# Optimization experiments

Measured on AMD Instinct MI355X. Metric: run time of the kernel, lower is better.

The kernel has to match this reference:

```python
import jax, jax.numpy as jnp
import numpy as np

N, E, NFEAT, NHID, NCLASS = 50000, 800000, 8, 128, 112
SMOOTH = 0.5          # smoo init arg
NEG_SLOPE_ATT = 0.2   # LeakyReLU slope inside sparse attention (SpGAT convention)
NEG_SLOPE_OUT = 0.01  # F.leaky_relu default in the outer loop
EPS = 1e-16


def setup_inputs() -> dict:
    key = jax.random.key(0)
    ks = jax.random.split(key, 12)
    g = lambda k, shape, s=0.1: jax.random.normal(k, shape, dtype=jnp.float32) * s
    return {
        "x": jax.random.normal(ks[0], (N, NFEAT), dtype=jnp.float32),
        "edge_index": jax.random.randint(ks[1], (2, E), 0, N, dtype=jnp.int64) if jax.config.jax_enable_x64 else jax.random.randint(ks[1], (2, E), 0, N, dtype=jnp.int32),
        "edge_weight": jax.random.uniform(ks[2], (E,), dtype=jnp.float32),
        # ScattterAttentionLayer 1: nfeat -> nhid (weight W, attention vector a split into src/dst halves)
        "W1": g(ks[3], (NFEAT, NHID)),
        "a1_src": g(ks[4], (NHID,)),
        "a1_dst": g(ks[5], (NHID,)),
        # ScattterAttentionLayer 2: nhid -> nhid
        "W2": g(ks[6], (NHID, NHID)),
        "a2_src": g(ks[7], (NHID,)),
        "a2_dst": g(ks[8], (NHID,)),
        # shared BatchNorm1d(nhid)
        "gamma": jnp.ones((NHID,), jnp.float32),
        "beta": jnp.zeros((NHID,), jnp.float32),
        # GC_withres: nhid -> nclass
        "Wg": g(ks[9], (NHID, NCLASS)),
        "bg": jnp.zeros((NCLASS,), jnp.float32),
    }


def scatter_attention(h_in, W, a_src, a_dst, src, dst):
    """Sparse GAT-style scatter attention (SpGraphAttentionLayer math).
    score_ij = exp(-leakyrelu(a_src.h_i + a_dst.h_j)); softmax-normalized per dst node."""
    h = h_in @ W                                   # [N, F]
    f_src = h @ a_src                              # [N]
    f_dst = h @ a_dst                              # [N]
    e = jnp.exp(-jax.nn.leaky_relu(f_src[src] + f_dst[dst], NEG_SLOPE_ATT))  # [E]
    denom = jax.ops.segment_sum(e, dst, num_segments=N) + EPS                # [N]
    num = jax.ops.segment_sum(e[:, None] * h[src], dst, num_segments=N)      # [N, F]
    return num / denom[:, None]


def batchnorm(x, gamma, beta):
    mu = x.mean(axis=0)
    var = x.var(axis=0)
    return (x - mu) * jax.lax.rsqrt(var + 1e-5) * gamma + beta


def reference(x, edge_index, edge_weight, W1, a1_src, a1_dst, W2, a2_src, a2_dst, gamma, beta, Wg, bg):
    src, dst = edge_index[0], edge_index[1]
    # conv loop (nlayers=3 -> two ScattterAttentionLayer convs), shared bn1, leaky_relu; dropout=identity (eval)
    h = scatter_attention(x, W1, a1_src, a1_dst, src, dst)
    h = jax.nn.leaky_relu(batchnorm(h, gamma, beta), NEG_SLOPE_OUT)
    h = scatter_attention(h, W2, a2_src, a2_dst, src, dst)
    h = jax.nn.leaky_relu(batchnorm(h, gamma, beta), NEG_SLOPE_OUT)
    # GC_withres: spmm((smooth*A + I)/(1+smooth), h @ Wg) + bias
    support = h @ Wg                               # [N, nclass]
    w = (SMOOTH / (1.0 + SMOOTH)) * edge_weight    # [E]
    agg = jax.ops.segment_sum(w[:, None] * support[src], dst, num_segments=N)
    return agg + support / (1.0 + SMOOTH) + bg
```

## Files before the change

kernel.cpp:

```cpp
#include <hip/hip_runtime.h>
#include <hip/hip_bf16.h>

#define N_NODES 50000
#define N_EDGES 800000
#define NFEAT   8
#define NHID    128
#define NCLASS  112
#define SEG_EPS 1e-16f
#define BN_EPS  1e-5f
#define CAP     64
#define MACRO_TILES 782
#define STAT_ROWS 50
#define STAT_BLOCKS 1000
#define NODE_RANGE 6250
#define FILL_CHUNK 2048
#define FILL_CHUNKS 391

typedef __hip_bfloat16 bf16;
typedef __attribute__((ext_vector_type(8))) short short8;
typedef __attribute__((ext_vector_type(4))) float f32x4;

__device__ __forceinline__ float bfbits2f(unsigned int lo16) {
    union { unsigned int u; float f; } c; c.u = lo16 << 16; return c.f;
}

__global__ __launch_bounds__(256)
void k_fill_bucket(const int* __restrict__ src, const int* __restrict__ dst,
                   const float* __restrict__ ewt,
                   int* __restrict__ cnt, unsigned int* __restrict__ bucket) {
    const int range = blockIdx.x & 7;
    const int chunk = blockIdx.x >> 3;
    const int lo = range * NODE_RANGE, hi = lo + NODE_RANGE;
    const int e0 = chunk * FILL_CHUNK + threadIdx.x;
#pragma unroll
    for (int i = 0; i < 8; i++) {
        int e = e0 + i * 256;
        if (e >= N_EDGES) break;
        int d = dst[e];
        if (d < lo || d >= hi) continue;
        int slot = atomicAdd(&cnt[d], 1);
        if (slot < CAP) {
            unsigned int iw = (unsigned int)(ewt[e] * 32767.f + 0.5f);
            bucket[d * CAP + slot] = ((unsigned int)src[e] << 15) | iw;
        }
    }
}

__global__ __launch_bounds__(256)
void k_sort_bucket(const int* __restrict__ cnt, unsigned int* __restrict__ bucket) {
    int d = blockIdx.x * 4 + (threadIdx.x >> 6);
    int lane = threadIdx.x & 63;
    int deg = min(cnt[d], CAP);
    unsigned int v = (lane < deg) ? bucket[d * CAP + lane] : 0xFFFFFFFFu;
#pragma unroll
    for (int k = 2; k <= 64; k <<= 1) {
#pragma unroll
        for (int s = k >> 1; s > 0; s >>= 1) {
            unsigned int o = (unsigned int)__shfl_xor((int)v, s);
            bool keepmin = ((lane & s) == 0) == ((lane & k) == 0);
            v = keepmin ? min(v, o) : max(v, o);
        }
    }
    if (lane < deg) bucket[d * CAP + lane] = v;
}

__global__ void k_w1proj(const float* __restrict__ W1,
                         const float* __restrict__ a1s, const float* __restrict__ a1d,
                         float* __restrict__ w1s, float* __restrict__ w1d) {
    int w = threadIdx.x >> 6, lane = threadIdx.x & 63;
    int k = w & 7;
    const float* a = (w < 8) ? a1s : a1d;
    float v = W1[k * NHID + lane] * a[lane] + W1[k * NHID + 64 + lane] * a[64 + lane];
#pragma unroll
    for (int off = 32; off > 0; off >>= 1) v += __shfl_down(v, off);
    if (lane == 0) ((w < 8) ? w1s : w1d)[k] = v;
}

__global__ void k_fsfd(const float* __restrict__ x,
                       const float* __restrict__ w1s, const float* __restrict__ w1d,
                       float* __restrict__ fs, float* __restrict__ fd) {
    int i = blockIdx.x * 256 + threadIdx.x;
    if (i >= N_NODES) return;
    const float4 x0 = ((const float4*)x)[i * 2];
    const float4 x1 = ((const float4*)x)[i * 2 + 1];
    fs[i] = x0.x*w1s[0] + x0.y*w1s[1] + x0.z*w1s[2] + x0.w*w1s[3]
          + x1.x*w1s[4] + x1.y*w1s[5] + x1.z*w1s[6] + x1.w*w1s[7];
    fd[i] = x0.x*w1d[0] + x0.y*w1d[1] + x0.z*w1d[2] + x0.w*w1d[3]
          + x1.x*w1d[4] + x1.y*w1d[5] + x1.z*w1d[6] + x1.w*w1d[7];
}

__global__ void k_gather_x(const int* __restrict__ cnt, const unsigned int* __restrict__ bucket,
                           const float* __restrict__ fs, const float* __restrict__ fd,
                           const float* __restrict__ x, float* __restrict__ xaggn) {
    int d = blockIdx.x * 4 + (threadIdx.x >> 6);
    int lane = threadIdx.x & 63;
    int col = lane & 7, eslot = lane >> 3;
    int dg = min(cnt[d], CAP);
    float fdd = fd[d];
    float acc = 0.f, den = 0.f;
    for (int base = 0; base < dg; base += 8) {
        int e = base + eslot;
        if (e < dg) {
            int s = bucket[d * CAP + e] >> 15;
            float f = fs[s] + fdd;
            float lr = f > 0.f ? f : 0.2f * f;
            float c = __expf(-lr);
            den += c;
            acc += c * x[s * NFEAT + col];
        }
    }
#pragma unroll
    for (int off = 8; off < 64; off <<= 1) {
        acc += __shfl_xor(acc, off);
        den += __shfl_xor(den, off);
    }
    if (eslot == 0) xaggn[d * NFEAT + col] = acc / (den + SEG_EPS);
}

__global__ __launch_bounds__(256)
void k_y1_gemm(const float* __restrict__ xaggn, const float* __restrict__ W1,
               bf16* __restrict__ y1, float* __restrict__ Psum, float* __restrict__ Psq) {
    int t = threadIdx.x;
    int r = t >> 7, j = t & 127;
    float w[NFEAT];
#pragma unroll
    for (int k = 0; k < NFEAT; k++) w[k] = W1[k * NHID + j];
    float ls = 0.f, lq = 0.f;
    for (int row = blockIdx.x * 2 + r; row < N_NODES; row += gridDim.x * 2) {
        const float4 x0 = ((const float4*)xaggn)[row * 2];
        const float4 x1 = ((const float4*)xaggn)[row * 2 + 1];
        float v = x0.x*w[0] + x0.y*w[1] + x0.z*w[2] + x0.w*w[3]
                + x1.x*w[4] + x1.y*w[5] + x1.z*w[6] + x1.w*w[7];
        y1[(size_t)row * NHID + j] = __float2bfloat16(v);
        ls += v; lq += v * v;
    }
    __shared__ float sbuf[256];
    sbuf[t] = ls; __syncthreads();
    if (r == 0) Psum[blockIdx.x * 128 + j] = sbuf[j] + sbuf[j + 128];
    __syncthreads();
    sbuf[t] = lq; __syncthreads();
    if (r == 0) Psq[blockIdx.x * 128 + j] = sbuf[j] + sbuf[j + 128];
}

__global__ __launch_bounds__(128)
void k_bn_stats_part(const bf16* __restrict__ y,
                     float* __restrict__ Psum, float* __restrict__ Psq) {
    int j = threadIdx.x;
    int i0 = blockIdx.x * STAT_ROWS;
    float ls = 0.f, lq = 0.f;
    for (int i = i0; i < i0 + STAT_ROWS; i++) {
        float v = __bfloat162float(y[(size_t)i * NHID + j]);
        ls += v; lq += v * v;
    }
    Psum[blockIdx.x * 128 + j] = ls;
    Psq[blockIdx.x * 128 + j] = lq;
}

__global__ __launch_bounds__(256)
void k_reduce_a(const float* __restrict__ Psum, const float* __restrict__ Psq,
                int nIn, int chunk,
                float* __restrict__ Qsum, float* __restrict__ Qsq) {
    int j = threadIdx.x & 127;
    int h = threadIdx.x >> 7;
    int u = blockIdx.x * 2 + h;
    int b0 = u * chunk, b1 = min(b0 + chunk, nIn);
    float s = 0.f, q = 0.f;
#pragma unroll 8
    for (int b = b0; b < b1; b++) {
        s += Psum[b * 128 + j];
        q += Psq[b * 128 + j];
    }
    Qsum[u * 128 + j] = s;
    Qsq[u * 128 + j] = q;
}

__global__ __launch_bounds__(512)
void k_reduce_b(const float* __restrict__ Qsum, const float* __restrict__ Qsq,
                const float* __restrict__ gamma, const float* __restrict__ beta,
                float* __restrict__ scale, float* __restrict__ shift) {
    int j = threadIdx.x & 127;
    int g = threadIdx.x >> 7;
    float s = 0.f, q = 0.f;
#pragma unroll
    for (int u = g * 8; u < g * 8 + 8; u++) {
        s += Qsum[u * 128 + j];
        q += Qsq[u * 128 + j];
    }
    __shared__ float Ls[4][128], Lq[4][128];
    Ls[g][j] = s; Lq[g][j] = q;
    __syncthreads();
    if (g == 0) {
        float st = ((Ls[0][j] + Ls[1][j]) + Ls[2][j]) + Ls[3][j];
        float qt = ((Lq[0][j] + Lq[1][j]) + Lq[2][j]) + Lq[3][j];
        float mu = st * (1.f / N_NODES);
        float var = qt * (1.f / N_NODES) - mu * mu;
        float rs = rsqrtf(var + BN_EPS);
        float ga = gamma[j];
        scale[j] = rs * ga;
        shift[j] = beta[j] - mu * rs * ga;
    }
}

__global__ void k_w2proj(const float* __restrict__ W2,
                         const float* __restrict__ as_, const float* __restrict__ ad_,
                         float* __restrict__ ws_, float* __restrict__ wd_) {
    int k = blockIdx.x, n = threadIdx.x;
    float w = W2[k * NHID + n];
    float vs = w * as_[n], vd = w * ad_[n];
#pragma unroll
    for (int off = 32; off > 0; off >>= 1) { vs += __shfl_down(vs, off); vd += __shfl_down(vd, off); }
    __shared__ float ps[2], pd[2];
    if ((n & 63) == 0) { ps[n >> 6] = vs; pd[n >> 6] = vd; }
    __syncthreads();
    if (n == 0) { ws_[k] = ps[0] + ps[1]; wd_[k] = pd[0] + pd[1]; }
}

template<int NCV, bool ATT>
__global__ __launch_bounds__(256)
void k_gemm_mfma(const bf16* __restrict__ Yin,
                 const float* __restrict__ scale, const float* __restrict__ shift,
                 const float* __restrict__ W,
                 bf16* __restrict__ hout,
                 const float* __restrict__ w2s, const float* __restrict__ w2d,
                 float* __restrict__ fs, float* __restrict__ fd) {
    constexpr int NT = NCV / 16;
    __shared__ bf16 Wt[128 * 136];
    __shared__ bf16 At[64 * 136];
    const int t = threadIdx.x;
    for (int idx = t; idx < 128 * NCV; idx += 256) {
        int k = idx / NCV, n = idx - k * NCV;
        Wt[n * 136 + k] = __float2bfloat16(W[idx]);
    }
    const int p  = t & 63;
    const int rg = t >> 6;
    const float sc0 = scale[2*p],   sh0 = shift[2*p];
    const float sc1 = scale[2*p+1], sh1 = shift[2*p+1];
    float ws0, ws1, wd0, wd1;
    if (ATT) { ws0 = w2s[2*p]; ws1 = w2s[2*p+1]; wd0 = w2d[2*p]; wd1 = w2d[2*p+1]; }
    const int lane = t & 63;
    const int m16 = lane & 15;
    const int g = lane >> 4;
    __syncthreads();

    for (int mt = blockIdx.x; mt < MACRO_TILES; mt += gridDim.x) {
        const int row0 = mt * 64;
#pragma unroll
        for (int i2 = 0; i2 < 16; i2++) {
            int row = rg + i2 * 4;
            int grow = row0 + row;
            unsigned int u = (grow < N_NODES) ? ((const unsigned int*)Yin)[(size_t)grow * 64 + p] : 0u;
            float v0 = bfbits2f(u & 0xFFFF) * sc0 + sh0; v0 = v0 > 0.f ? v0 : 0.01f * v0;
            float v1 = bfbits2f(u >> 16)    * sc1 + sh1; v1 = v1 > 0.f ? v1 : 0.01f * v1;
            union { unsigned int u; bf16 b[2]; } pk;
            pk.b[0] = __float2bfloat16(v0);
            pk.b[1] = __float2bfloat16(v1);
            *(unsigned int*)&At[row * 136 + 2 * p] = pk.u;
            if (ATT) {
                float vs = v0 * ws0 + v1 * ws1;
                float vd = v0 * wd0 + v1 * wd1;
#pragma unroll
                for (int off = 32; off > 0; off >>= 1) {
                    vs += __shfl_xor(vs, off);
                    vd += __shfl_xor(vd, off);
                }
                if (p == 0 && grow < N_NODES) { fs[grow] = vs; fd[grow] = vd; }
            }
        }
        __syncthreads();
        f32x4 acc[NT];
#pragma unroll
        for (int c = 0; c < NT; c++) acc[c] = (f32x4){0.f, 0.f, 0.f, 0.f};
#pragma unroll
        for (int kk = 0; kk < 4; kk++) {
            short8 af = *(const short8*)&At[(rg * 16 + m16) * 136 + kk * 32 + g * 8];
#pragma unroll
            for (int c = 0; c < NT; c++) {
                short8 bfr = *(const short8*)&Wt[(c * 16 + m16) * 136 + kk * 32 + g * 8];
                acc[c] = __builtin_amdgcn_mfma_f32_16x16x32_bf16(af, bfr, acc[c], 0, 0, 0);
            }
        }
        const int orow = row0 + rg * 16 + g * 4;
#pragma unroll
        for (int c = 0; c < NT; c++) {
#pragma unroll
            for (int r = 0; r < 4; r++) {
                int grow = orow + r;
                if (grow < N_NODES)
                    hout[(size_t)grow * NCV + c * 16 + m16] = __float2bfloat16(acc[c][r]);
            }
        }
        __syncthreads();
    }
}

__global__ __launch_bounds__(256)
void k_gather_attn_bf(const int* __restrict__ cnt, const unsigned int* __restrict__ bucket,
                      const float* __restrict__ fs, const float* __restrict__ fd,
                      const bf16* __restrict__ h, bf16* __restrict__ y) {
    int q = threadIdx.x >> 6;
    int j = threadIdx.x & 63;
    int d = blockIdx.x * 4 + q;
    __shared__ int s_idx[4][CAP];
    __shared__ float s_e[4][CAP];
    int deg = min(cnt[d], CAP);
    float fdd = fd[d];
    if (j < deg) {
        int s = bucket[d * CAP + j] >> 15;
        float f = fs[s] + fdd;
        float lr = f > 0.f ? f : 0.2f * f;
        s_idx[q][j] = s;
        s_e[q][j] = __expf(-lr);
    }
    __syncthreads();
    float n0 = 0.f, n1 = 0.f, den = 0.f;
#pragma unroll 4
    for (int k = 0; k < deg; k++) {
        float e = s_e[q][k];
        unsigned int u = *(const unsigned int*)&h[(size_t)s_idx[q][k] * NHID + 2 * j];
        den += e;
        n0 += e * bfbits2f(u & 0xFFFF);
        n1 += e * bfbits2f(u >> 16);
    }
    float rs = 1.f / (den + SEG_EPS);
    union { unsigned int u; bf16 b[2]; } pk;
    pk.b[0] = __float2bfloat16(n0 * rs);
    pk.b[1] = __float2bfloat16(n1 * rs);
    ((unsigned int*)y)[(size_t)d * 64 + j] = pk.u;
}

__global__ __launch_bounds__(256)
void k_gather_out_bf(const int* __restrict__ cnt, const unsigned int* __restrict__ bucket,
                     const bf16* __restrict__ sup, const float* __restrict__ bg,
                     float* __restrict__ out) {
    int q = threadIdx.x >> 6;
    int j = threadIdx.x & 63;
    int d = blockIdx.x * 4 + q;
    __shared__ int s_idx[4][CAP];
    __shared__ float s_w[4][CAP];
    int deg = min(cnt[d], CAP);
    if (j < deg) {
        unsigned int b = bucket[d * CAP + j];
        s_idx[q][j] = b >> 15;
        s_w[q][j] = (float)(b & 0x7FFF) * (1.f / (32767.f * 3.f));
    }
    __syncthreads();
    if (j >= NCLASS / 2) return;
    float a0 = 0.f, a1 = 0.f;
#pragma unroll 4
    for (int k = 0; k < deg; k++) {
        float w = s_w[q][k];
        unsigned int u = *(const unsigned int*)&sup[(size_t)s_idx[q][k] * NCLASS + 2 * j];
        a0 += w * bfbits2f(u & 0xFFFF);
        a1 += w * bfbits2f(u >> 16);
    }
    unsigned int us = *(const unsigned int*)&sup[(size_t)d * NCLASS + 2 * j];
    float2 o;
    o.x = a0 + bfbits2f(us & 0xFFFF) * (2.f / 3.f) + bg[2 * j];
    o.y = a1 + bfbits2f(us >> 16)    * (2.f / 3.f) + bg[2 * j + 1];
    *(float2*)&out[(size_t)d * NCLASS + 2 * j] = o;
}

extern "C" void kernel_launch(void* const* d_in, const int* in_sizes, int n_in,
                              void* d_out, int out_size, void* d_ws, size_t ws_size,
                              hipStream_t stream) {
    const float* x    = (const float*)d_in[0];
    const int*   ei   = (const int*)d_in[1];
    const float* ewt  = (const float*)d_in[2];
    const float* W1   = (const float*)d_in[3];
    const float* a1s  = (const float*)d_in[4];
    const float* a1d  = (const float*)d_in[5];
    const float* W2   = (const float*)d_in[6];
    const float* a2s  = (const float*)d_in[7];
    const float* a2d  = (const float*)d_in[8];
    const float* gam  = (const float*)d_in[9];
    const float* bet  = (const float*)d_in[10];
    const float* Wg   = (const float*)d_in[11];
    const float* bg   = (const float*)d_in[12];
    float* out = (float*)d_out;

    const int* src = ei;
    const int* dst = ei + N_EDGES;

    float* ws    = (float*)d_ws;
    bf16*  Yb    = (bf16*)ws;
    bf16*  Hb    = (bf16*)(ws + 3203072);
    unsigned int* bucket = (unsigned int*)(ws + 6403072);
    float* xagg  = ws + 9603072;
    float* fs    = ws + 10003072;
    float* fd    = ws + 10053072;
    int*   cnt   = (int*)(ws + 10103072);
    float* scale = ws + 10153072;
    float* shift = scale + 128;
    float* w1s   = shift + 128;
    float* w1d   = w1s + 8;
    float* w2s   = w1d + 8;
    float* w2d   = w2s + 128;
    float* Psum  = ws + 10153600;
    float* Psq   = Psum + 128000;
    float* Qsum  = Psq + 128000;
    float* Qsq   = Qsum + 4096;

    hipMemsetAsync(cnt, 0, (size_t)N_NODES * 4, stream);
    k_fill_bucket<<<FILL_CHUNKS * 8, 256, 0, stream>>>(src, dst, ewt, cnt, bucket);
    k_sort_bucket<<<N_NODES / 4, 256, 0, stream>>>(cnt, bucket);

    k_w1proj<<<1, 1024, 0, stream>>>(W1, a1s, a1d, w1s, w1d);
    k_fsfd<<<(N_NODES + 255) / 256, 256, 0, stream>>>(x, w1s, w1d, fs, fd);
    k_gather_x<<<N_NODES / 4, 256, 0, stream>>>(cnt, bucket, fs, fd, x, xagg);
    k_y1_gemm<<<256, 256, 0, stream>>>(xagg, W1, Yb, Psum, Psq);
    k_reduce_a<<<16, 256, 0, stream>>>(Psum, Psq, 256, 8, Qsum, Qsq);
    k_reduce_b<<<1, 512, 0, stream>>>(Qsum, Qsq, gam, bet, scale, shift);

    k_w2proj<<<128, 128, 0, stream>>>(W2, a2s, a2d, w2s, w2d);
    k_gemm_mfma<128, true><<<MACRO_TILES, 256, 0, stream>>>(Yb, scale, shift, W2, Hb,
                                                            w2s, w2d, fs, fd);
    k_gather_attn_bf<<<N_NODES / 4, 256, 0, stream>>>(cnt, bucket, fs, fd, Hb, Yb);
    k_bn_stats_part<<<STAT_BLOCKS, 128, 0, stream>>>(Yb, Psum, Psq);
    k_reduce_a<<<16, 256, 0, stream>>>(Psum, Psq, STAT_BLOCKS, 32, Qsum, Qsq);
    k_reduce_b<<<1, 512, 0, stream>>>(Qsum, Qsq, gam, bet, scale, shift);

    k_gemm_mfma<112, false><<<MACRO_TILES, 256, 0, stream>>>(Yb, scale, shift, Wg, Hb,
                                                             nullptr, nullptr, nullptr, nullptr);
    k_gather_out_bf<<<N_NODES / 4, 256, 0, stream>>>(cnt, bucket, Hb, bg, out);
}
```

Measured before the change: 328.3 us.

## Fuse tiny projection/BN-finalize kernels into consumers and split gather edges across half-waves

The W1 attention projection now runs inside k_fsfd and the BatchNorm finalize (k_reduce_b) runs inside each GEMM block's prologue, which removes three small serial launches. The attention and output gather kernels now have each half-wave take alternate edges with 4-wide bf16 loads, then combine the halves with a cross-lane shuffle. This gives more memory-level parallelism per node. In exchange, every GEMM block redundantly reads the 32x128 partial stats and every fsfd block recomputes the W1 projection.

Result: slower. 345.3 us (+5.2%).

```diff
diff --git a/kernel.cpp b/kernel.cpp
--- a/kernel.cpp
+++ b/kernel.cpp
@@ -64,22 +64,32 @@
     if (lane < deg) bucket[d * CAP + lane] = v;
 }
 
-__global__ void k_w1proj(const float* __restrict__ W1,
-                         const float* __restrict__ a1s, const float* __restrict__ a1d,
-                         float* __restrict__ w1s, float* __restrict__ w1d) {
-    int w = threadIdx.x >> 6, lane = threadIdx.x & 63;
-    int k = w & 7;
-    const float* a = (w < 8) ? a1s : a1d;
-    float v = W1[k * NHID + lane] * a[lane] + W1[k * NHID + 64 + lane] * a[64 + lane];
-#pragma unroll
-    for (int off = 32; off > 0; off >>= 1) v += __shfl_down(v, off);
-    if (lane == 0) ((w < 8) ? w1s : w1d)[k] = v;
-}
-
-__global__ void k_fsfd(const float* __restrict__ x,
-                       const float* __restrict__ w1s, const float* __restrict__ w1d,
-                       float* __restrict__ fs, float* __restrict__ fd) {
-    int i = blockIdx.x * 256 + threadIdx.x;
+__global__ __launch_bounds__(256)
+void k_fsfd(const float* __restrict__ W1,
+            const float* __restrict__ a1s, const float* __restrict__ a1d,
+            const float* __restrict__ x,
+            float* __restrict__ fs, float* __restrict__ fd) {
+    __shared__ float ps[8][32], pd_[8][32];
+    __shared__ float w1s[8], w1d[8];
+    int t = threadIdx.x;
+    int k = t & 7, seg = t >> 3;
+    float accs = 0.f, accd = 0.f;
+#pragma unroll
+    for (int n = seg * 4; n < seg * 4 + 4; n++) {
+        float w = W1[k * NHID + n];
+        accs += w * a1s[n];
+        accd += w * a1d[n];
+    }
+    ps[k][seg] = accs; pd_[k][seg] = accd;
+    __syncthreads();
+    if (t < 8) {
+        float vs = 0.f, vd = 0.f;
+#pragma unroll 8
+        for (int i = 0; i < 32; i++) { vs += ps[t][i]; vd += pd_[t][i]; }
+        w1s[t] = vs; w1d[t] = vd;
+    }
+    __syncthreads();
+    int i = blockIdx.x * 256 + t;
     if (i >= N_NODES) return;
     const float4 x0 = ((const float4*)x)[i * 2];
     const float4 x1 = ((const float4*)x)[i * 2 + 1];
@@ -174,33 +184,6 @@
     Qsq[u * 128 + j] = q;
 }
 
-__global__ __launch_bounds__(512)
-void k_reduce_b(const float* __restrict__ Qsum, const float* __restrict__ Qsq,
-                const float* __restrict__ gamma, const float* __restrict__ beta,
-                float* __restrict__ scale, float* __restrict__ shift) {
-    int j = threadIdx.x & 127;
-    int g = threadIdx.x >> 7;
-    float s = 0.f, q = 0.f;
-#pragma unroll
-    for (int u = g * 8; u < g * 8 + 8; u++) {
-        s += Qsum[u * 128 + j];
-        q += Qsq[u * 128 + j];
-    }
-    __shared__ float Ls[4][128], Lq[4][128];
-    Ls[g][j] = s; Lq[g][j] = q;
-    __syncthreads();
-    if (g == 0) {
-        float st = ((Ls[0][j] + Ls[1][j]) + Ls[2][j]) + Ls[3][j];
-        float qt = ((Lq[0][j] + Lq[1][j]) + Lq[2][j]) + Lq[3][j];
-        float mu = st * (1.f / N_NODES);
-        float var = qt * (1.f / N_NODES) - mu * mu;
-        float rs = rsqrtf(var + BN_EPS);
-        float ga = gamma[j];
-        scale[j] = rs * ga;
-        shift[j] = beta[j] - mu * rs * ga;
-    }
-}
-
 __global__ void k_w2proj(const float* __restrict__ W2,
                          const float* __restrict__ as_, const float* __restrict__ ad_,
                          float* __restrict__ ws_, float* __restrict__ wd_) {
@@ -218,7 +201,8 @@
 template<int NCV, bool ATT>
 __global__ __launch_bounds__(256)
 void k_gemm_mfma(const bf16* __restrict__ Yin,
-                 const float* __restrict__ scale, const float* __restrict__ shift,
+                 const float* __restrict__ Qsum, const float* __restrict__ Qsq,
+                 const float* __restrict__ gamma, const float* __restrict__ beta,
                  const float* __restrict__ W,
                  bf16* __restrict__ hout,
                  const float* __restrict__ w2s, const float* __restrict__ w2d,
@@ -233,8 +217,20 @@
     }
     const int p  = t & 63;
     const int rg = t >> 6;
-    const float sc0 = scale[2*p],   sh0 = shift[2*p];
-    const float sc1 = scale[2*p+1], sh1 = shift[2*p+1];
+    float s0 = 0.f, q0 = 0.f, s1 = 0.f, q1 = 0.f;
+#pragma unroll 8
+    for (int u = 0; u < 32; u++) {
+        s0 += Qsum[u * 128 + 2 * p];     s1 += Qsum[u * 128 + 2 * p + 1];
+        q0 += Qsq[u * 128 + 2 * p];      q1 += Qsq[u * 128 + 2 * p + 1];
+    }
+    float mu0 = s0 * (1.f / N_NODES);
+    float rs0 = rsqrtf(q0 * (1.f / N_NODES) - mu0 * mu0 + BN_EPS);
+    float g0  = gamma[2 * p];
+    const float sc0 = rs0 * g0, sh0 = beta[2 * p] - mu0 * rs0 * g0;
+    float mu1 = s1 * (1.f / N_NODES);
+    float rs1 = rsqrtf(q1 * (1.f / N_NODES) - mu1 * mu1 + BN_EPS);
+    float g1  = gamma[2 * p + 1];
+    const float sc1 = rs1 * g1, sh1 = beta[2 * p + 1] - mu1 * rs1 * g1;
     float ws0, ws1, wd0, wd1;
     if (ATT) { ws0 = w2s[2*p]; ws1 = w2s[2*p+1]; wd0 = w2d[2*p]; wd1 = w2d[2*p+1]; }
     const int lane = t & 63;
@@ -298,34 +294,39 @@
                       const float* __restrict__ fs, const float* __restrict__ fd,
                       const bf16* __restrict__ h, bf16* __restrict__ y) {
     int q = threadIdx.x >> 6;
-    int j = threadIdx.x & 63;
+    int lane = threadIdx.x & 63;
     int d = blockIdx.x * 4 + q;
     __shared__ int s_idx[4][CAP];
     __shared__ float s_e[4][CAP];
     int deg = min(cnt[d], CAP);
     float fdd = fd[d];
-    if (j < deg) {
-        int s = bucket[d * CAP + j] >> 15;
+    if (lane < deg) {
+        int s = bucket[d * CAP + lane] >> 15;
         float f = fs[s] + fdd;
         float lr = f > 0.f ? f : 0.2f * f;
-        s_idx[q][j] = s;
-        s_e[q][j] = __expf(-lr);
-    }
-    __syncthreads();
-    float n0 = 0.f, n1 = 0.f, den = 0.f;
-#pragma unroll 4
-    for (int k = 0; k < deg; k++) {
+        s_idx[q][lane] = s;
+        s_e[q][lane] = __expf(-lr);
+    }
+    __syncthreads();
+    int half = lane >> 5, j4 = lane & 31;
+    float n0 = 0.f, n1 = 0.f, n2 = 0.f, n3 = 0.f, den = 0.f;
+    for (int k = half; k < deg; k += 2) {
         float e = s_e[q][k];
-        unsigned int u = *(const unsigned int*)&h[(size_t)s_idx[q][k] * NHID + 2 * j];
+        const uint2 u = *(const uint2*)&h[(size_t)s_idx[q][k] * NHID + 4 * j4];
         den += e;
-        n0 += e * bfbits2f(u & 0xFFFF);
-        n1 += e * bfbits2f(u >> 16);
-    }
-    float rs = 1.f / (den + SEG_EPS);
-    union { unsigned int u; bf16 b[2]; } pk;
-    pk.b[0] = __float2bfloat16(n0 * rs);
-    pk.b[1] = __float2bfloat16(n1 * rs);
-    ((unsigned int*)y)[(size_t)d * 64 + j] = pk.u;
+        n0 += e * bfbits2f(u.x & 0xFFFF); n1 += e * bfbits2f(u.x >> 16);
+        n2 += e * bfbits2f(u.y & 0xFFFF); n3 += e * bfbits2f(u.y >> 16);
+    }
+    n0 += __shfl_xor(n0, 32); n1 += __shfl_xor(n1, 32);
+    n2 += __shfl_xor(n2, 32); n3 += __shfl_xor(n3, 32);
+    den += __shfl_xor(den, 32);
+    if (half == 0) {
+        float rs = 1.f / (den + SEG_EPS);
+        union { uint2 u; bf16 b[4]; } pk;
+        pk.b[0] = __float2bfloat16(n0 * rs); pk.b[1] = __float2bfloat16(n1 * rs);
+        pk.b[2] = __float2bfloat16(n2 * rs); pk.b[3] = __float2bfloat16(n3 * rs);
+        ((uint2*)y)[(size_t)d * 32 + j4] = pk.u;
+    }
 }
 
 __global__ __launch_bounds__(256)
@@ -333,31 +334,38 @@
                      const bf16* __restrict__ sup, const float* __restrict__ bg,
                      float* __restrict__ out) {
     int q = threadIdx.x >> 6;
-    int j = threadIdx.x & 63;
+    int lane = threadIdx.x & 63;
     int d = blockIdx.x * 4 + q;
     __shared__ int s_idx[4][CAP];
     __shared__ float s_w[4][CAP];
     int deg = min(cnt[d], CAP);
-    if (j < deg) {
-        unsigned int b = bucket[d * CAP + j];
-        s_idx[q][j] = b >> 15;
-        s_w[q][j] = (float)(b & 0x7FFF) * (1.f / (32767.f * 3.f));
-    }
-    __syncthreads();
-    if (j >= NCLASS / 2) return;
-    float a0 = 0.f, a1 = 0.f;
-#pragma unroll 4
-    for (int k = 0; k < deg; k++) {
-        float w = s_w[q][k];
-        unsigned int u = *(const unsigned int*)&sup[(size_t)s_idx[q][k] * NCLASS + 2 * j];
-        a0 += w * bfbits2f(u & 0xFFFF);
-        a1 += w * bfbits2f(u >> 16);
-    }
-    unsigned int us = *(const unsigned int*)&sup[(size_t)d * NCLASS + 2 * j];
-    float2 o;
-    o.x = a0 + bfbits2f(us & 0xFFFF) * (2.f / 3.f) + bg[2 * j];
-    o.y = a1 + bfbits2f(us >> 16)    * (2.f / 3.f) + bg[2 * j + 1];
-    *(float2*)&out[(size_t)d * NCLASS + 2 * j] = o;
+    if (lane < deg) {
+        unsigned int b = bucket[d * CAP + lane];
+        s_idx[q][lane] = b >> 15;
+        s_w[q][lane] = (float)(b & 0x7FFF) * (1.f / (32767.f * 3.f));
+    }
+    __syncthreads();
+    int half = lane >> 5, j4 = lane & 31;
+    float a0 = 0.f, a1 = 0.f, a2 = 0.f, a3 = 0.f;
+    if (j4 < 28) {
+        for (int k = half; k < deg; k += 2) {
+            float w = s_w[q][k];
+            const uint2 u = *(const uint2*)&sup[(size_t)s_idx[q][k] * NCLASS + 4 * j4];
+            a0 += w * bfbits2f(u.x & 0xFFFF); a1 += w * bfbits2f(u.x >> 16);
+            a2 += w * bfbits2f(u.y & 0xFFFF); a3 += w * bfbits2f(u.y >> 16);
+        }
+    }
+    a0 += __shfl_xor(a0, 32); a1 += __shfl_xor(a1, 32);
+    a2 += __shfl_xor(a2, 32); a3 += __shfl_xor(a3, 32);
+    if (half == 0 && j4 < 28) {
+        const uint2 us = *(const uint2*)&sup[(size_t)d * NCLASS + 4 * j4];
+        float4 o;
+        o.x = a0 + bfbits2f(us.x & 0xFFFF) * (2.f / 3.f) + bg[4 * j4];
+        o.y = a1 + bfbits2f(us.x >> 16)    * (2.f / 3.f) + bg[4 * j4 + 1];
+        o.z = a2 + bfbits2f(us.y & 0xFFFF) * (2.f / 3.f) + bg[4 * j4 + 2];
+        o.w = a3 + bfbits2f(us.y >> 16)    * (2.f / 3.f) + bg[4 * j4 + 3];
+        *(float4*)&out[(size_t)d * NCLASS + 4 * j4] = o;
+    }
 }
 
 extern "C" void kernel_launch(void* const* d_in, const int* in_sizes, int n_in,
@@ -389,11 +397,7 @@
     float* fs    = ws + 10003072;
     float* fd    = ws + 10053072;
     int*   cnt   = (int*)(ws + 10103072);
-    float* scale = ws + 10153072;
-    float* shift = scale + 128;
-    float* w1s   = shift + 128;
-    float* w1d   = w1s + 8;
-    float* w2s   = w1d + 8;
+    float* w2s   = ws + 10153072;
     float* w2d   = w2s + 128;
     float* Psum  = ws + 10153600;
     float* Psq   = Psum + 128000;
@@ -404,22 +408,19 @@
     k_fill_bucket<<<FILL_CHUNKS * 8, 256, 0, stream>>>(src, dst, ewt, cnt, bucket);
     k_sort_bucket<<<N_NODES / 4, 256, 0, stream>>>(cnt, bucket);
 
-    k_w1proj<<<1, 1024, 0, stream>>>(W1, a1s, a1d, w1s, w1d);
-    k_fsfd<<<(N_NODES + 255) / 256, 256, 0, stream>>>(x, w1s, w1d, fs, fd);
+    k_fsfd<<<(N_NODES + 255) / 256, 256, 0, stream>>>(W1, a1s, a1d, x, fs, fd);
     k_gather_x<<<N_NODES / 4, 256, 0, stream>>>(cnt, bucket, fs, fd, x, xagg);
     k_y1_gemm<<<256, 256, 0, stream>>>(xagg, W1, Yb, Psum, Psq);
     k_reduce_a<<<16, 256, 0, stream>>>(Psum, Psq, 256, 8, Qsum, Qsq);
-    k_reduce_b<<<1, 512, 0, stream>>>(Qsum, Qsq, gam, bet, scale, shift);
 
     k_w2proj<<<128, 128, 0, stream>>>(W2, a2s, a2d, w2s, w2d);
-    k_gemm_mfma<128, true><<<MACRO_TILES, 256, 0, stream>>>(Yb, scale, shift, W2, Hb,
+    k_gemm_mfma<128, true><<<MACRO_TILES, 256, 0, stream>>>(Yb, Qsum, Qsq, gam, bet, W2, Hb,
                                                             w2s, w2d, fs, fd);
     k_gather_attn_bf<<<N_NODES / 4, 256, 0, stream>>>(cnt, bucket, fs, fd, Hb, Yb);
     k_bn_stats_part<<<STAT_BLOCKS, 128, 0, stream>>>(Yb, Psum, Psq);
     k_reduce_a<<<16, 256, 0, stream>>>(Psum, Psq, STAT_BLOCKS, 32, Qsum, Qsq);
-    k_reduce_b<<<1, 512, 0, stream>>>(Qsum, Qsq, gam, bet, scale, shift);
-
-    k_gemm_mfma<112, false><<<MACRO_TILES, 256, 0, stream>>>(Yb, scale, shift, Wg, Hb,
+
+    k_gemm_mfma<112, false><<<MACRO_TILES, 256, 0, stream>>>(Yb, Qsum, Qsq, gam, bet, Wg, Hb,
                                                              nullptr, nullptr, nullptr, nullptr);
     k_gather_out_bf<<<N_NODES / 4, 256, 0, stream>>>(cnt, bucket, Hb, bg, out);
 }
```
